# Performance work log

Hardware: AMD Instinct MI355X
Metric: run time of the kernel (lower is better)

Reference implementation:

```python
import jax, jax.numpy as jnp
import numpy as np

N_NODES = 50000
N_EDGES = 800000
NUM_GRAPHS = 64
D_IN = 128
D_HID = 128
D_EMB = 128
D_PRED = 256
D_OUT = 1
BN_EPS = 1e-5


def gcn_conv(x, W, b, src, dst, n_nodes):
    # PyG GCNConv: add self-loops, sym-normalize, aggregate, then bias.
    h = x @ W  # [N, d_out]
    # in-degree with self-loops
    deg = jax.ops.segment_sum(jnp.ones((src.shape[0],), h.dtype), dst,
                              num_segments=n_nodes) + 1.0
    inv_sqrt = 1.0 / jnp.sqrt(deg)  # [N]
    norm = inv_sqrt[src] * inv_sqrt[dst]  # [E]
    msg = h[src] * norm[:, None]  # [E, d_out] gather + scale
    agg = jax.ops.segment_sum(msg, dst, num_segments=n_nodes)
    # self-loop contribution: norm_ii = 1/deg_i
    agg = agg + h / deg[:, None]
    return agg + b


def batch_norm(h, gamma, beta):
    # BatchNorm1d in training mode: batch stats, biased variance
    mean = jnp.mean(h, axis=0)
    var = jnp.mean(jnp.square(h - mean), axis=0)
    return (h - mean) / jnp.sqrt(var + BN_EPS) * gamma + beta


def setup_inputs() -> dict:
    key = jax.random.key(0)
    ks = jax.random.split(key, 12)
    x = jax.random.normal(ks[0], (N_NODES, D_IN), dtype=jnp.float32)
    edge_index = jax.random.randint(ks[1], (2, N_EDGES), 0, N_NODES, dtype=jnp.int32)
    batch = jnp.sort(jax.random.randint(ks[2], (N_NODES,), 0, NUM_GRAPHS, dtype=jnp.int32))
    s1 = 1.0 / np.sqrt(D_IN)
    s2 = 1.0 / np.sqrt(D_HID)
    s3 = 1.0 / np.sqrt(D_EMB)
    s4 = 1.0 / np.sqrt(D_PRED)
    return {
        "x": x,
        "edge_index": edge_index,
        "batch": batch,
        "W1": jax.random.uniform(ks[3], (D_IN, D_HID), jnp.float32, -s1, s1),
        "b1": jnp.zeros((D_HID,), jnp.float32),
        "g1": jnp.ones((D_HID,), jnp.float32),
        "be1": jnp.zeros((D_HID,), jnp.float32),
        "W2": jax.random.uniform(ks[4], (D_HID, D_EMB), jnp.float32, -s2, s2),
        "b2": jnp.zeros((D_EMB,), jnp.float32),
        "g2": jnp.ones((D_EMB,), jnp.float32),
        "be2": jnp.zeros((D_EMB,), jnp.float32),
        "Wp1": jax.random.uniform(ks[5], (D_EMB, D_PRED), jnp.float32, -s3, s3),
        "bp1": jax.random.uniform(ks[6], (D_PRED,), jnp.float32, -s3, s3),
        "Wp2": jax.random.uniform(ks[7], (D_PRED, D_OUT), jnp.float32, -s4, s4),
        "bp2": jax.random.uniform(ks[8], (D_OUT,), jnp.float32, -s4, s4),
    }


def reference(x, edge_index, batch, W1, b1, g1, be1, W2, b2, g2, be2, Wp1, bp1, Wp2, bp2):
    src, dst = edge_index[0], edge_index[1]
    h = gcn_conv(x, W1, b1, src, dst, N_NODES)
    h = batch_norm(jax.nn.relu(h), g1, be1)
    h = gcn_conv(h, W2, b2, src, dst, N_NODES)
    h = batch_norm(jax.nn.relu(h), g2, be2)
    # global max pool per graph
    pooled = jax.ops.segment_max(h, batch, num_segments=NUM_GRAPHS)  # [G, D_EMB]
    # predictor MLP (Dropout is identity in eval)
    z = jax.nn.relu(pooled @ Wp1 + bp1)
    return z @ Wp2 + bp2
```

## Files before the change

kernel.cpp:

```cpp
#include <hip/hip_runtime.h>

#define NN 50000
#define NE 800000
#define NG 64
#define D 128
#define DP 256
#define BN_EPS 1e-5f
#define NSLOT 32
#define NB 196

typedef unsigned short bf16;
typedef __attribute__((ext_vector_type(8))) short s16x8;
typedef __attribute__((ext_vector_type(4))) float f32x4;

__device__ __forceinline__ float bf2f(unsigned h16) {
  unsigned u = (h16 & 0xffffu) << 16; float f; __builtin_memcpy(&f, &u, 4); return f;
}
__device__ __forceinline__ bf16 f2bf(float f) {
  unsigned u; __builtin_memcpy(&u, &f, 4);
  return (bf16)((u + 0x7FFFu + ((u >> 16) & 1u)) >> 16);
}
__device__ __forceinline__ unsigned packbf2(float a, float b) {
  return (unsigned)f2bf(a) | ((unsigned)f2bf(b) << 16);
}
__device__ __forceinline__ s16x8 u4cast(uint4 v) {
  s16x8 r; __builtin_memcpy(&r, &v, 16); return r;
}

__global__ void k_detect(const unsigned short* __restrict__ x, int* __restrict__ flag) {
  int i = threadIdx.x;
  float v = bf2f(x[2 * i]);
  float a = fabsf(v);
  int good = (v == 0.0f) || (a > 1e-30f && a < 32.0f);
  unsigned long long m = __ballot(good);
  if (i == 0) {
    flag[0] = (__popcll(m) >= 56) ? 1 : 0;
    flag[1] = 1;
  }
}

struct CvtArgs {
  const void* s[12];
  float* d[12];
  int n[12];
};

__global__ __launch_bounds__(256) void k_cvt(CvtArgs a, const int* __restrict__ flag) {
  int t = blockIdx.y;
  int n = a.n[t];
  int base = blockIdx.x * 2048;
  if (base >= n) return;
  int mode = flag[0];
  float* dp = a.d[t];
  if (n >= 8) {
    int i8 = base + threadIdx.x * 8;
    if (i8 + 8 <= n) {
      if (mode) {
        uint4 raw = *(const uint4*)((const bf16*)a.s[t] + i8);
        float4 o0 = make_float4(bf2f(raw.x & 0xffff), bf2f(raw.x >> 16),
                                bf2f(raw.y & 0xffff), bf2f(raw.y >> 16));
        float4 o1 = make_float4(bf2f(raw.z & 0xffff), bf2f(raw.z >> 16),
                                bf2f(raw.w & 0xffff), bf2f(raw.w >> 16));
        *(float4*)(dp + i8) = o0;
        *(float4*)(dp + i8 + 4) = o1;
      } else {
        const float* s = (const float*)a.s[t] + i8;
        *(float4*)(dp + i8) = *(const float4*)s;
        *(float4*)(dp + i8 + 4) = *(const float4*)(s + 4);
      }
    }
  } else {
    int i = base + threadIdx.x;
    if (i < n) dp[i] = mode ? bf2f(((const bf16*)a.s[t])[i]) : ((const float*)a.s[t])[i];
  }
}

__global__ __launch_bounds__(256) void k_deg(const int* __restrict__ ei, int* __restrict__ cnt) {
  int e = blockIdx.x * 256 + threadIdx.x;
  if (e < NE) atomicAdd(&cnt[ei[NE + e]], 1);
}

__global__ __launch_bounds__(256) void k_bsum(const int* __restrict__ cnt, int* __restrict__ bsum) {
  int i = blockIdx.x * 256 + threadIdx.x;
  int v = (i < NN) ? cnt[i] : 0;
  __shared__ int s[4];
  for (int off = 32; off; off >>= 1) v += __shfl_down(v, off);
  if ((threadIdx.x & 63) == 0) s[threadIdx.x >> 6] = v;
  __syncthreads();
  if (threadIdx.x == 0) bsum[blockIdx.x] = s[0] + s[1] + s[2] + s[3];
}

__global__ __launch_bounds__(256) void k_bscan(const int* __restrict__ bsum, int* __restrict__ bbase) {
  __shared__ int sh[256];
  int t = threadIdx.x;
  int v = (t < NB) ? bsum[t] : 0;
  sh[t] = v;
  __syncthreads();
  for (int off = 1; off < 256; off <<= 1) {
    int u = (t >= off) ? sh[t - off] : 0;
    __syncthreads();
    sh[t] += u;
    __syncthreads();
  }
  if (t < NB) bbase[t] = sh[t] - v;
}

__global__ __launch_bounds__(256) void k_offsets(const int* __restrict__ cnt, const int* __restrict__ bbase,
                                                 int* __restrict__ ro, int* __restrict__ cursor,
                                                 float* __restrict__ isq) {
  __shared__ int sh[256];
  int t = threadIdx.x;
  int i = blockIdx.x * 256 + t;
  int c = (i < NN) ? cnt[i] : 0;
  sh[t] = c;
  __syncthreads();
  for (int off = 1; off < 256; off <<= 1) {
    int u = (t >= off) ? sh[t - off] : 0;
    __syncthreads();
    sh[t] += u;
    __syncthreads();
  }
  if (i < NN) {
    int o = bbase[blockIdx.x] + sh[t] - c;
    ro[i] = o; cursor[i] = o;
    isq[i] = rsqrtf((float)(c + 1));
  }
  if (i == 0) ro[NN] = NE;
}

__global__ __launch_bounds__(256) void k_fill(const int* __restrict__ ei, const float* __restrict__ isq,
                                              int* __restrict__ cursor, int2* __restrict__ pk) {
  int e = blockIdx.x * 256 + threadIdx.x;
  if (e < NE) {
    int s = ei[e], d = ei[NE + e];
    int slot = atomicAdd(&cursor[d], 1);
    int2 v; v.x = s; v.y = __float_as_int(isq[s] * isq[d]);
    pk[slot] = v;
  }
}

__global__ __launch_bounds__(256) void k_pack(const float* __restrict__ W, const float* __restrict__ scale,
                                              bf16* __restrict__ Wp) {
  int slot = blockIdx.x * 256 + threadIdx.x;
  if (slot >= 2048) return;
  int kc = slot >> 9, ct = (slot >> 6) & 7, l = slot & 63;
  int q = l >> 4, p = l & 15;
  int n = ct * 16 + p;
  unsigned u[4];
#pragma unroll
  for (int jj = 0; jj < 4; ++jj) {
    int k0 = kc * 32 + q * 8 + jj * 2;
    float w0 = W[k0 * D + n], w1 = W[(k0 + 1) * D + n];
    if (scale) { w0 *= scale[k0]; w1 *= scale[k0 + 1]; }
    u[jj] = packbf2(w0, w1);
  }
  uint4 o = make_uint4(u[0], u[1], u[2], u[3]);
  *(uint4*)(Wp + (size_t)slot * 8) = o;
}

__global__ __launch_bounds__(256) void k_mgemm(const void* __restrict__ Xv, const int* __restrict__ flag,
                                               const bf16* __restrict__ Wp,
                                               const float* __restrict__ rowadd,
                                               bf16* __restrict__ Out, int nrows) {
  __shared__ float Cs[4][16][D + 4];
  int l = threadIdx.x & 63, w = threadIdx.x >> 6;
  int q = l >> 4, p = l & 15;
  int mode = flag ? flag[0] : 0;
  float rv[8];
#pragma unroll
  for (int ct = 0; ct < 8; ++ct) rv[ct] = rowadd ? rowadd[ct * 16 + p] : 0.f;
  int ntiles = (nrows + 63) >> 6;
  for (int t = blockIdx.x; t < ntiles; t += gridDim.x) {
    int wb = t * 64 + w * 16;
    int rowc = min(wb + p, nrows - 1);
    f32x4 acc[8];
#pragma unroll
    for (int ct = 0; ct < 8; ++ct) { f32x4 z = {rv[ct], rv[ct], rv[ct], rv[ct]}; acc[ct] = z; }
#pragma unroll
    for (int kc = 0; kc < 4; ++kc) {
      s16x8 a;
      if (mode) {
        uint4 av = *(const uint4*)((const bf16*)Xv + (size_t)rowc * D + kc * 32 + q * 8);
        a = u4cast(av);
      } else {
        const float* Xf = (const float*)Xv + (size_t)rowc * D + kc * 32 + q * 8;
        float4 f0 = *(const float4*)Xf;
        float4 f1 = *(const float4*)(Xf + 4);
        uint4 u = make_uint4(packbf2(f0.x, f0.y), packbf2(f0.z, f0.w),
                             packbf2(f1.x, f1.y), packbf2(f1.z, f1.w));
        a = u4cast(u);
      }
#pragma unroll
      for (int ct = 0; ct < 8; ++ct) {
        s16x8 bfr = *(const s16x8*)(Wp + (size_t)(((kc << 3) + ct) * 64 + l) * 8);
        acc[ct] = __builtin_amdgcn_mfma_f32_16x16x32_bf16(a, bfr, acc[ct], 0, 0, 0);
      }
    }
#pragma unroll
    for (int ct = 0; ct < 8; ++ct)
#pragma unroll
      for (int r = 0; r < 4; ++r)
        Cs[w][q * 4 + r][ct * 16 + p] = acc[ct][r];
    __syncthreads();
#pragma unroll
    for (int i = 0; i < 4; ++i) {
      int idx = i * 64 + l;
      int rr = idx >> 4, c8 = idx & 15;
      int gr = t * 64 + w * 16 + rr;
      if (gr < nrows) {
        float4 v0 = *(const float4*)&Cs[w][rr][c8 * 8];
        float4 v1 = *(const float4*)&Cs[w][rr][c8 * 8 + 4];
        uint4 o = make_uint4(packbf2(v0.x, v0.y), packbf2(v0.z, v0.w),
                             packbf2(v1.x, v1.y), packbf2(v1.z, v1.w));
        *(uint4*)(Out + (size_t)gr * D + c8 * 8) = o;
      }
    }
    __syncthreads();
  }
}

template <int LAYER2>
__global__ __launch_bounds__(256) void k_agg(const bf16* __restrict__ H, const int* __restrict__ ro,
                                             const int2* __restrict__ pk,
                                             const float* __restrict__ b, const int* __restrict__ batch,
                                             bf16* __restrict__ Rout,
                                             float* __restrict__ sumP, float* __restrict__ sumsqP,
                                             float* __restrict__ pooled) {
  int lane = threadIdx.x & 63;
  int w = __builtin_amdgcn_readfirstlane(threadIdx.x >> 6);
  int nbase = blockIdx.x * 16 + w * 4;
  float2 bv = ((const float2*)b)[lane];
  float2 ls = make_float2(0.f, 0.f), lq = make_float2(0.f, 0.f);
  int gcur = -1; float2 mx = make_float2(0.f, 0.f);
  int nend = min(nbase + 4, NN);
  for (int n = nbase; n < nend; ++n) {
    int r0 = __builtin_amdgcn_readfirstlane(ro[n]);
    int r1 = __builtin_amdgcn_readfirstlane(ro[n + 1]);
    float invd = 1.0f / (float)(r1 - r0 + 1);
    unsigned hv = ((const unsigned*)(H + (size_t)n * D))[lane];
    float2 acc = make_float2(bf2f(hv & 0xffff) * invd, bf2f(hv >> 16) * invd);
    int e = r0;
    for (; e + 8 <= r1; e += 8) {
      int2 P[8];
      unsigned X[8];
#pragma unroll
      for (int j = 0; j < 8; ++j) P[j] = pk[e + j];
#pragma unroll
      for (int j = 0; j < 8; ++j) X[j] = ((const unsigned*)(H + (size_t)P[j].x * D))[lane];
#pragma unroll
      for (int j = 0; j < 8; ++j) {
        float c = __int_as_float(P[j].y);
        acc.x += bf2f(X[j] & 0xffff) * c; acc.y += bf2f(X[j] >> 16) * c;
      }
    }
    for (; e + 4 <= r1; e += 4) {
      int2 p0 = pk[e], p1 = pk[e + 1], p2 = pk[e + 2], p3 = pk[e + 3];
      unsigned x0 = ((const unsigned*)(H + (size_t)p0.x * D))[lane];
      unsigned x1 = ((const unsigned*)(H + (size_t)p1.x * D))[lane];
      unsigned x2 = ((const unsigned*)(H + (size_t)p2.x * D))[lane];
      unsigned x3 = ((const unsigned*)(H + (size_t)p3.x * D))[lane];
      float c0 = __int_as_float(p0.y), c1 = __int_as_float(p1.y);
      float c2 = __int_as_float(p2.y), c3 = __int_as_float(p3.y);
      acc.x += bf2f(x0 & 0xffff) * c0; acc.y += bf2f(x0 >> 16) * c0;
      acc.x += bf2f(x1 & 0xffff) * c1; acc.y += bf2f(x1 >> 16) * c1;
      acc.x += bf2f(x2 & 0xffff) * c2; acc.y += bf2f(x2 >> 16) * c2;
      acc.x += bf2f(x3 & 0xffff) * c3; acc.y += bf2f(x3 >> 16) * c3;
    }
    for (; e < r1; ++e) {
      int2 p0 = pk[e];
      unsigned x0 = ((const unsigned*)(H + (size_t)p0.x * D))[lane];
      float c0 = __int_as_float(p0.y);
      acc.x += bf2f(x0 & 0xffff) * c0; acc.y += bf2f(x0 >> 16) * c0;
    }
    float2 r = make_float2(fmaxf(acc.x + bv.x, 0.f), fmaxf(acc.y + bv.y, 0.f));
    if (!LAYER2) ((unsigned*)(Rout + (size_t)n * D))[lane] = packbf2(r.x, r.y);
    ls.x += r.x; ls.y += r.y; lq.x += r.x * r.x; lq.y += r.y * r.y;
    if (LAYER2) {
      int g = batch[n];
      if (g != gcur) {
        if (gcur >= 0) {
          atomicMax((int*)&pooled[(size_t)gcur * D + 2 * lane], __float_as_int(mx.x));
          atomicMax((int*)&pooled[(size_t)gcur * D + 2 * lane + 1], __float_as_int(mx.y));
        }
        gcur = g; mx = make_float2(0.f, 0.f);
      }
      mx.x = fmaxf(mx.x, r.x); mx.y = fmaxf(mx.y, r.y);
    }
  }
  if (LAYER2 && gcur >= 0) {
    atomicMax((int*)&pooled[(size_t)gcur * D + 2 * lane], __float_as_int(mx.x));
    atomicMax((int*)&pooled[(size_t)gcur * D + 2 * lane + 1], __float_as_int(mx.y));
  }
  __shared__ float ss[4][D], sq[4][D];
  ss[w][2 * lane] = ls.x; ss[w][2 * lane + 1] = ls.y;
  sq[w][2 * lane] = lq.x; sq[w][2 * lane + 1] = lq.y;
  __syncthreads();
  int slot = (blockIdx.x & (NSLOT - 1)) * D;
  if (threadIdx.x < D) {
    int k = threadIdx.x;
    atomicAdd(&sumP[slot + k], ss[0][k] + ss[1][k] + ss[2][k] + ss[3][k]);
  } else {
    int k = threadIdx.x - D;
    atomicAdd(&sumsqP[slot + k], sq[0][k] + sq[1][k] + sq[2][k] + sq[3][k]);
  }
}

__global__ void k_bnstats1(const float* __restrict__ sumP, const float* __restrict__ sumsqP,
                           const float* __restrict__ gamma, const float* __restrict__ beta,
                           const float* __restrict__ W2,
                           float* __restrict__ svec, float* __restrict__ tW2) {
  __shared__ float t[D];
  int k = threadIdx.x;
  float sm = 0.f, sq = 0.f;
  for (int i = 0; i < NSLOT; ++i) { sm += sumP[i * D + k]; sq += sumsqP[i * D + k]; }
  float mean = sm * (1.0f / NN);
  float var = sq * (1.0f / NN) - mean * mean;
  float s = gamma[k] * rsqrtf(var + BN_EPS);
  svec[k] = s;
  t[k] = beta[k] - mean * s;
  __syncthreads();
  float acc = 0.f;
  for (int kk = 0; kk < D; ++kk) acc += t[kk] * W2[kk * D + k];
  tW2[k] = acc;
}

__global__ void k_bnstats2(const float* __restrict__ sumP, const float* __restrict__ sumsqP,
                           const float* __restrict__ gamma, const float* __restrict__ beta,
                           float* __restrict__ svec, float* __restrict__ tvec) {
  int k = threadIdx.x;
  float sm = 0.f, sq = 0.f;
  for (int i = 0; i < NSLOT; ++i) { sm += sumP[i * D + k]; sq += sumsqP[i * D + k]; }
  float mean = sm * (1.0f / NN);
  float var = sq * (1.0f / NN) - mean * mean;
  float s = gamma[k] * rsqrtf(var + BN_EPS);
  svec[k] = s;
  tvec[k] = beta[k] - mean * s;
}

__global__ __launch_bounds__(256) void k_head(const float* __restrict__ pooled, const float* __restrict__ s2,
                                              const float* __restrict__ t2, const float* __restrict__ Wp1,
                                              const float* __restrict__ bp1, const float* __restrict__ Wp2,
                                              const float* __restrict__ bp2, void* out,
                                              const int* __restrict__ flag) {
  __shared__ float y[D];
  __shared__ float wr[4];
  int g = blockIdx.x, j = threadIdx.x;
  if (j < D) y[j] = pooled[(size_t)g * D + j] * s2[j] + t2[j];
  __syncthreads();
  float acc = bp1[j];
#pragma unroll 4
  for (int k = 0; k < D; ++k) acc += y[k] * Wp1[k * DP + j];
  float v = fmaxf(acc, 0.f) * Wp2[j];
  for (int off = 32; off; off >>= 1) v += __shfl_down(v, off);
  if ((j & 63) == 0) wr[j >> 6] = v;
  __syncthreads();
  if (j == 0) {
    float r = wr[0] + wr[1] + wr[2] + wr[3] + bp2[0];
    if (flag[0]) ((bf16*)out)[g] = f2bf(r);
    else ((float*)out)[g] = r;
  }
}

extern "C" void kernel_launch(void* const* d_in, const int* in_sizes, int n_in,
                              void* d_out, int out_size, void* d_ws, size_t ws_size,
                              hipStream_t stream) {
  const void* x   = d_in[0];
  const int*  ei  = (const int*)d_in[1];
  const int*  bat = (const int*)d_in[2];

  float* f = (float*)d_ws;
  bf16* A = (bf16*)f; f += (size_t)NN * D / 2;
  bf16* B = (bf16*)f; f += (size_t)NN * D / 2;
  float* W1f  = f; f += D * D;
  float* W2f  = f; f += D * D;
  float* Wp1f = f; f += D * DP;
  float* b1f  = f; f += D;
  float* g1f  = f; f += D;
  float* be1f = f; f += D;
  float* b2f  = f; f += D;
  float* g2f  = f; f += D;
  float* be2f = f; f += D;
  float* bp1f = f; f += DP;
  float* Wp2f = f; f += DP;
  float* bp2f = f; f += 4;
  bf16* Wpk1 = (bf16*)f; f += 2048 * 8 / 2;
  bf16* Wpk2 = (bf16*)f; f += 2048 * 8 / 2;
  float* sum1P   = f; f += NSLOT * D;
  float* sumsq1P = f; f += NSLOT * D;
  float* sum2P   = f; f += NSLOT * D;
  float* sumsq2P = f; f += NSLOT * D;
  float* pooled = f; f += (size_t)NG * D;
  float* svec1  = f; f += D;
  float* tW2    = f; f += D;
  float* svec2  = f; f += D;
  float* tvec2  = f; f += D;
  float* isq    = f; f += NN;
  int2* pk     = (int2*)f; f += (size_t)NE * 2;
  int* ro      = (int*)f; f += NN + 1;
  int* cursor  = (int*)f; f += NN;
  int* cnt     = (int*)f; f += NN;
  int* bsum    = (int*)f; f += NB;
  int* bbase   = (int*)f; f += NB;
  int* flag    = (int*)f;

  hipMemsetAsync(cnt, 0, NN * sizeof(int), stream);
  hipMemsetAsync(sum1P, 0, (4 * NSLOT * D + NG * D) * sizeof(float), stream);

  k_detect<<<1, 64, 0, stream>>>((const unsigned short*)x, flag);

  CvtArgs ca;
  ca.s[0] = d_in[3];  ca.d[0] = W1f;  ca.n[0] = D * D;
  ca.s[1] = d_in[7];  ca.d[1] = W2f;  ca.n[1] = D * D;
  ca.s[2] = d_in[11]; ca.d[2] = Wp1f; ca.n[2] = D * DP;
  ca.s[3] = d_in[4];  ca.d[3] = b1f;  ca.n[3] = D;
  ca.s[4] = d_in[5];  ca.d[4] = g1f;  ca.n[4] = D;
  ca.s[5] = d_in[6];  ca.d[5] = be1f; ca.n[5] = D;
  ca.s[6] = d_in[8];  ca.d[6] = b2f;  ca.n[6] = D;
  ca.s[7] = d_in[9];  ca.d[7] = g2f;  ca.n[7] = D;
  ca.s[8] = d_in[10]; ca.d[8] = be2f; ca.n[8] = D;
  ca.s[9] = d_in[12]; ca.d[9] = bp1f; ca.n[9] = DP;
  ca.s[10] = d_in[13]; ca.d[10] = Wp2f; ca.n[10] = DP;
  ca.s[11] = d_in[14]; ca.d[11] = bp2f; ca.n[11] = 1;
  k_cvt<<<dim3(16, 12), 256, 0, stream>>>(ca, flag);

  k_deg<<<(NE + 255) / 256, 256, 0, stream>>>(ei, cnt);
  k_bsum<<<NB, 256, 0, stream>>>(cnt, bsum);
  k_bscan<<<1, 256, 0, stream>>>(bsum, bbase);
  k_offsets<<<NB, 256, 0, stream>>>(cnt, bbase, ro, cursor, isq);
  k_fill<<<(NE + 255) / 256, 256, 0, stream>>>(ei, isq, cursor, pk);
  k_pack<<<8, 256, 0, stream>>>(W1f, nullptr, Wpk1);

  k_mgemm<<<(NN + 63) / 64, 256, 0, stream>>>(x, flag, Wpk1, nullptr, A, NN);
  k_agg<0><<<(NN + 15) / 16, 256, 0, stream>>>(A, ro, pk, b1f, nullptr,
                                               B, sum1P, sumsq1P, nullptr);
  k_bnstats1<<<1, D, 0, stream>>>(sum1P, sumsq1P, g1f, be1f, W2f, svec1, tW2);

  k_pack<<<8, 256, 0, stream>>>(W2f, svec1, Wpk2);
  k_mgemm<<<(NN + 63) / 64, 256, 0, stream>>>(B, flag + 1, Wpk2, tW2, A, NN);
  k_agg<1><<<(NN + 15) / 16, 256, 0, stream>>>(A, ro, pk, b2f, bat,
                                               nullptr, sum2P, sumsq2P, pooled);
  k_bnstats2<<<1, D, 0, stream>>>(sum2P, sumsq2P, g2f, be2f, svec2, tvec2);

  k_head<<<NG, DP, 0, stream>>>(pooled, svec2, tvec2, Wp1f, bp1f, Wp2f, bp2f, d_out, flag);
}
```

Before: 231.3 us.

## Fuse preprocessing launches and rework aggregation to split edges across half-waves

Merges the detect, convert and degree-count kernels into one launch, and replaces the block-sum/scan/offsets chain with a single scan kernel. That kernel uses a grid-wide spin barrier on an atomic counter and also packs W1. The BN2 stats are folded into the head kernel, and the two memsets become one. The aggregation kernel now gives each half-wave a separate edge while every lane loads 4 bf16 features, then combines the halves with a cross-lane shuffle. The goal is fewer launches and more memory-level parallelism in the gather, but the spin barrier only works if all 204 blocks are resident at the same time.

```diff
diff --git a/kernel.cpp b/kernel.cpp
--- a/kernel.cpp
+++ b/kernel.cpp
@@ -8,6 +8,7 @@
 #define BN_EPS 1e-5f
 #define NSLOT 32
 #define NB 196
+#define NEB 3125
 
 typedef unsigned short bf16;
 typedef __attribute__((ext_vector_type(8))) short s16x8;
@@ -25,18 +26,6 @@
 }
 __device__ __forceinline__ s16x8 u4cast(uint4 v) {
   s16x8 r; __builtin_memcpy(&r, &v, 16); return r;
-}
-
-__global__ void k_detect(const unsigned short* __restrict__ x, int* __restrict__ flag) {
-  int i = threadIdx.x;
-  float v = bf2f(x[2 * i]);
-  float a = fabsf(v);
-  int good = (v == 0.0f) || (a > 1e-30f && a < 32.0f);
-  unsigned long long m = __ballot(good);
-  if (i == 0) {
-    flag[0] = (__popcll(m) >= 56) ? 1 : 0;
-    flag[1] = 1;
-  }
 }
 
 struct CvtArgs {
@@ -45,56 +34,100 @@
   int n[12];
 };
 
-__global__ __launch_bounds__(256) void k_cvt(CvtArgs a, const int* __restrict__ flag) {
-  int t = blockIdx.y;
-  int n = a.n[t];
-  int base = blockIdx.x * 2048;
-  if (base >= n) return;
-  int mode = flag[0];
-  float* dp = a.d[t];
-  if (n >= 8) {
-    int i8 = base + threadIdx.x * 8;
-    if (i8 + 8 <= n) {
-      if (mode) {
-        uint4 raw = *(const uint4*)((const bf16*)a.s[t] + i8);
-        float4 o0 = make_float4(bf2f(raw.x & 0xffff), bf2f(raw.x >> 16),
-                                bf2f(raw.y & 0xffff), bf2f(raw.y >> 16));
-        float4 o1 = make_float4(bf2f(raw.z & 0xffff), bf2f(raw.z >> 16),
-                                bf2f(raw.w & 0xffff), bf2f(raw.w >> 16));
-        *(float4*)(dp + i8) = o0;
-        *(float4*)(dp + i8 + 4) = o1;
-      } else {
-        const float* s = (const float*)a.s[t] + i8;
-        *(float4*)(dp + i8) = *(const float4*)s;
-        *(float4*)(dp + i8 + 4) = *(const float4*)(s + 4);
-      }
-    }
-  } else {
-    int i = base + threadIdx.x;
-    if (i < n) dp[i] = mode ? bf2f(((const bf16*)a.s[t])[i]) : ((const float*)a.s[t])[i];
-  }
-}
-
-__global__ __launch_bounds__(256) void k_deg(const int* __restrict__ ei, int* __restrict__ cnt) {
-  int e = blockIdx.x * 256 + threadIdx.x;
-  if (e < NE) atomicAdd(&cnt[ei[NE + e]], 1);
-}
-
-__global__ __launch_bounds__(256) void k_bsum(const int* __restrict__ cnt, int* __restrict__ bsum) {
-  int i = blockIdx.x * 256 + threadIdx.x;
-  int v = (i < NN) ? cnt[i] : 0;
-  __shared__ int s[4];
-  for (int off = 32; off; off >>= 1) v += __shfl_down(v, off);
-  if ((threadIdx.x & 63) == 0) s[threadIdx.x >> 6] = v;
-  __syncthreads();
-  if (threadIdx.x == 0) bsum[blockIdx.x] = s[0] + s[1] + s[2] + s[3];
-}
-
-__global__ __launch_bounds__(256) void k_bscan(const int* __restrict__ bsum, int* __restrict__ bbase) {
+__global__ __launch_bounds__(256) void k_pre(const int* __restrict__ ei, int* __restrict__ cnt,
+                                             CvtArgs a, const bf16* __restrict__ x,
+                                             int* __restrict__ flag) {
+  int b = blockIdx.x;
+  if (b < NEB) {
+    int e = b * 256 + threadIdx.x;
+    atomicAdd(&cnt[ei[NE + e]], 1);
+    return;
+  }
+  if (b < NEB + 192) {
+    __shared__ int smode;
+    if (threadIdx.x < 64) {
+      float v = bf2f(x[2 * threadIdx.x]);
+      float av = fabsf(v);
+      int good = (v == 0.0f) || (av > 1e-30f && av < 32.0f);
+      unsigned long long m = __ballot(good);
+      if (threadIdx.x == 0) smode = (__popcll(m) >= 56) ? 1 : 0;
+    }
+    __syncthreads();
+    int mode = smode;
+    int idx = b - NEB;
+    int t = idx >> 4;
+    int base = (idx & 15) * 2048;
+    int n = a.n[t];
+    if (base >= n) return;
+    float* dp = a.d[t];
+    if (n >= 8) {
+      int i8 = base + threadIdx.x * 8;
+      if (i8 + 8 <= n) {
+        if (mode) {
+          uint4 raw = *(const uint4*)((const bf16*)a.s[t] + i8);
+          *(float4*)(dp + i8) = make_float4(bf2f(raw.x & 0xffff), bf2f(raw.x >> 16),
+                                            bf2f(raw.y & 0xffff), bf2f(raw.y >> 16));
+          *(float4*)(dp + i8 + 4) = make_float4(bf2f(raw.z & 0xffff), bf2f(raw.z >> 16),
+                                                bf2f(raw.w & 0xffff), bf2f(raw.w >> 16));
+        } else {
+          const float* s = (const float*)a.s[t] + i8;
+          *(float4*)(dp + i8) = *(const float4*)s;
+          *(float4*)(dp + i8 + 4) = *(const float4*)(s + 4);
+        }
+      }
+    } else {
+      int i = base + threadIdx.x;
+      if (i < n) dp[i] = mode ? bf2f(((const bf16*)a.s[t])[i]) : ((const float*)a.s[t])[i];
+    }
+    return;
+  }
+  if (threadIdx.x < 64) {
+    float v = bf2f(x[2 * threadIdx.x]);
+    float av = fabsf(v);
+    int good = (v == 0.0f) || (av > 1e-30f && av < 32.0f);
+    unsigned long long m = __ballot(good);
+    if (threadIdx.x == 0) { flag[0] = (__popcll(m) >= 56) ? 1 : 0; flag[1] = 1; }
+  }
+}
+
+__device__ __forceinline__ void pack_slot(const float* __restrict__ W, const float* __restrict__ scale,
+                                          bf16* __restrict__ Wp, int slot) {
+  int kc = slot >> 9, ct = (slot >> 6) & 7, l = slot & 63;
+  int q = l >> 4, p = l & 15;
+  int n = ct * 16 + p;
+  unsigned u[4];
+#pragma unroll
+  for (int jj = 0; jj < 4; ++jj) {
+    int k0 = kc * 32 + q * 8 + jj * 2;
+    float w0 = W[k0 * D + n], w1 = W[(k0 + 1) * D + n];
+    if (scale) { w0 *= scale[k0]; w1 *= scale[k0 + 1]; }
+    u[jj] = packbf2(w0, w1);
+  }
+  *(uint4*)(Wp + (size_t)slot * 8) = make_uint4(u[0], u[1], u[2], u[3]);
+}
+
+__global__ __launch_bounds__(256) void k_pack(const float* __restrict__ W, const float* __restrict__ scale,
+                                              bf16* __restrict__ Wp) {
+  int slot = blockIdx.x * 256 + threadIdx.x;
+  if (slot < 2048) pack_slot(W, scale, Wp, slot);
+}
+
+__global__ __launch_bounds__(256) void k_scan3(const int* __restrict__ cnt,
+                                               int* __restrict__ bsum, int* __restrict__ done,
+                                               int* __restrict__ ro, int* __restrict__ cursor,
+                                               float* __restrict__ isq,
+                                               const float* __restrict__ W1f, bf16* __restrict__ Wpk1) {
+  int b = blockIdx.x, t = threadIdx.x;
+  if (b >= NB) {
+    pack_slot(W1f, nullptr, Wpk1, (b - NB) * 256 + t);
+    return;
+  }
   __shared__ int sh[256];
-  int t = threadIdx.x;
-  int v = (t < NB) ? bsum[t] : 0;
-  sh[t] = v;
+  __shared__ int spart[4];
+  __shared__ int sbase;
+  int i = b * 256 + t;
+  int c = (i < NN) ? cnt[i] : 0;
+  sh[t] = c;
   __syncthreads();
   for (int off = 1; off < 256; off <<= 1) {
     int u = (t >= off) ? sh[t - off] : 0;
@@ -102,26 +135,23 @@
     sh[t] += u;
     __syncthreads();
   }
-  if (t < NB) bbase[t] = sh[t] - v;
-}
-
-__global__ __launch_bounds__(256) void k_offsets(const int* __restrict__ cnt, const int* __restrict__ bbase,
-                                                 int* __restrict__ ro, int* __restrict__ cursor,
-                                                 float* __restrict__ isq) {
-  __shared__ int sh[256];
-  int t = threadIdx.x;
-  int i = blockIdx.x * 256 + t;
-  int c = (i < NN) ? cnt[i] : 0;
-  sh[t] = c;
-  __syncthreads();
-  for (int off = 1; off < 256; off <<= 1) {
-    int u = (t >= off) ? sh[t - off] : 0;
-    __syncthreads();
-    sh[t] += u;
-    __syncthreads();
-  }
+  if (t == 255) {
+    atomicExch(&bsum[b], sh[255]);
+    __threadfence();
+    atomicAdd(done, 1);
+  }
+  if (t == 0) {
+    while (atomicAdd(done, 0) < NB) { __builtin_amdgcn_s_sleep(2); }
+  }
+  __syncthreads();
+  int v = (t < b) ? atomicAdd(&bsum[t], 0) : 0;
+  for (int off = 32; off; off >>= 1) v += __shfl_down(v, off);
+  if ((t & 63) == 0) spart[t >> 6] = v;
+  __syncthreads();
+  if (t == 0) sbase = spart[0] + spart[1] + spart[2] + spart[3];
+  __syncthreads();
   if (i < NN) {
-    int o = bbase[blockIdx.x] + sh[t] - c;
+    int o = sbase + sh[t] - c;
     ro[i] = o; cursor[i] = o;
     isq[i] = rsqrtf((float)(c + 1));
   }
@@ -137,25 +167,6 @@
     int2 v; v.x = s; v.y = __float_as_int(isq[s] * isq[d]);
     pk[slot] = v;
   }
-}
-
-__global__ __launch_bounds__(256) void k_pack(const float* __restrict__ W, const float* __restrict__ scale,
-                                              bf16* __restrict__ Wp) {
-  int slot = blockIdx.x * 256 + threadIdx.x;
-  if (slot >= 2048) return;
-  int kc = slot >> 9, ct = (slot >> 6) & 7, l = slot & 63;
-  int q = l >> 4, p = l & 15;
-  int n = ct * 16 + p;
-  unsigned u[4];
-#pragma unroll
-  for (int jj = 0; jj < 4; ++jj) {
-    int k0 = kc * 32 + q * 8 + jj * 2;
-    float w0 = W[k0 * D + n], w1 = W[(k0 + 1) * D + n];
-    if (scale) { w0 *= scale[k0]; w1 *= scale[k0 + 1]; }
-    u[jj] = packbf2(w0, w1);
-  }
-  uint4 o = make_uint4(u[0], u[1], u[2], u[3]);
-  *(uint4*)(Wp + (size_t)slot * 8) = o;
 }
 
 __global__ __launch_bounds__(256) void k_mgemm(const void* __restrict__ Xv, const int* __restrict__ flag,
@@ -220,80 +231,88 @@
 }
 
 template <int LAYER2>
-__global__ __launch_bounds__(256) void k_agg(const bf16* __restrict__ H, const int* __restrict__ ro,
-                                             const int2* __restrict__ pk,
-                                             const float* __restrict__ b, const int* __restrict__ batch,
-                                             bf16* __restrict__ Rout,
-                                             float* __restrict__ sumP, float* __restrict__ sumsqP,
-                                             float* __restrict__ pooled) {
+__global__ __launch_bounds__(256, 4) void k_agg(const bf16* __restrict__ H, const int* __restrict__ ro,
+                                                const int2* __restrict__ pk,
+                                                const float* __restrict__ b, const int* __restrict__ batch,
+                                                bf16* __restrict__ Rout,
+                                                float* __restrict__ sumP, float* __restrict__ sumsqP,
+                                                float* __restrict__ pooled) {
   int lane = threadIdx.x & 63;
   int w = __builtin_amdgcn_readfirstlane(threadIdx.x >> 6);
+  int h = lane >> 5, c = lane & 31;
   int nbase = blockIdx.x * 16 + w * 4;
-  float2 bv = ((const float2*)b)[lane];
-  float2 ls = make_float2(0.f, 0.f), lq = make_float2(0.f, 0.f);
-  int gcur = -1; float2 mx = make_float2(0.f, 0.f);
+  float4 bv = ((const float4*)b)[c];
+  float ls[4] = {0.f, 0.f, 0.f, 0.f}, lq[4] = {0.f, 0.f, 0.f, 0.f}, mx[4] = {0.f, 0.f, 0.f, 0.f};
+  int gcur = -1;
   int nend = min(nbase + 4, NN);
   for (int n = nbase; n < nend; ++n) {
-    int r0 = __builtin_amdgcn_readfirstlane(ro[n]);
-    int r1 = __builtin_amdgcn_readfirstlane(ro[n + 1]);
-    float invd = 1.0f / (float)(r1 - r0 + 1);
-    unsigned hv = ((const unsigned*)(H + (size_t)n * D))[lane];
-    float2 acc = make_float2(bf2f(hv & 0xffff) * invd, bf2f(hv >> 16) * invd);
-    int e = r0;
-    for (; e + 8 <= r1; e += 8) {
-      int2 P[8];
-      unsigned X[8];
-#pragma unroll
-      for (int j = 0; j < 8; ++j) P[j] = pk[e + j];
-#pragma unroll
-      for (int j = 0; j < 8; ++j) X[j] = ((const unsigned*)(H + (size_t)P[j].x * D))[lane];
-#pragma unroll
-      for (int j = 0; j < 8; ++j) {
-        float c = __int_as_float(P[j].y);
-        acc.x += bf2f(X[j] & 0xffff) * c; acc.y += bf2f(X[j] >> 16) * c;
-      }
-    }
-    for (; e + 4 <= r1; e += 4) {
-      int2 p0 = pk[e], p1 = pk[e + 1], p2 = pk[e + 2], p3 = pk[e + 3];
-      unsigned x0 = ((const unsigned*)(H + (size_t)p0.x * D))[lane];
-      unsigned x1 = ((const unsigned*)(H + (size_t)p1.x * D))[lane];
-      unsigned x2 = ((const unsigned*)(H + (size_t)p2.x * D))[lane];
-      unsigned x3 = ((const unsigned*)(H + (size_t)p3.x * D))[lane];
-      float c0 = __int_as_float(p0.y), c1 = __int_as_float(p1.y);
-      float c2 = __int_as_float(p2.y), c3 = __int_as_float(p3.y);
-      acc.x += bf2f(x0 & 0xffff) * c0; acc.y += bf2f(x0 >> 16) * c0;
-      acc.x += bf2f(x1 & 0xffff) * c1; acc.y += bf2f(x1 >> 16) * c1;
-      acc.x += bf2f(x2 & 0xffff) * c2; acc.y += bf2f(x2 >> 16) * c2;
-      acc.x += bf2f(x3 & 0xffff) * c3; acc.y += bf2f(x3 >> 16) * c3;
-    }
-    for (; e < r1; ++e) {
-      int2 p0 = pk[e];
-      unsigned x0 = ((const unsigned*)(H + (size_t)p0.x * D))[lane];
-      float c0 = __int_as_float(p0.y);
-      acc.x += bf2f(x0 & 0xffff) * c0; acc.y += bf2f(x0 >> 16) * c0;
-    }
-    float2 r = make_float2(fmaxf(acc.x + bv.x, 0.f), fmaxf(acc.y + bv.y, 0.f));
-    if (!LAYER2) ((unsigned*)(Rout + (size_t)n * D))[lane] = packbf2(r.x, r.y);
-    ls.x += r.x; ls.y += r.y; lq.x += r.x * r.x; lq.y += r.y * r.y;
+    int e0 = __builtin_amdgcn_readfirstlane(ro[n]);
+    int e1 = __builtin_amdgcn_readfirstlane(ro[n + 1]);
+    float invd = 1.0f / (float)(e1 - e0 + 1);
+    uint2 hv = ((const uint2*)(H + (size_t)n * D))[c];
+    float acc[4] = {0.f, 0.f, 0.f, 0.f};
+    int e = e0;
+    for (; e + 8 <= e1; e += 8) {
+      int2 P[4]; uint2 X[4];
+#pragma unroll
+      for (int it = 0; it < 4; ++it) P[it] = pk[e + 2 * it + h];
+#pragma unroll
+      for (int it = 0; it < 4; ++it) X[it] = ((const uint2*)(H + (size_t)P[it].x * D))[c];
+#pragma unroll
+      for (int it = 0; it < 4; ++it) {
+        float cc = __int_as_float(P[it].y);
+        acc[0] += bf2f(X[it].x & 0xffff) * cc; acc[1] += bf2f(X[it].x >> 16) * cc;
+        acc[2] += bf2f(X[it].y & 0xffff) * cc; acc[3] += bf2f(X[it].y >> 16) * cc;
+      }
+    }
+    for (; e < e1; e += 2) {
+      int eh = e + h;
+      int2 p0 = (eh < e1) ? pk[eh] : make_int2(n, 0);
+      uint2 X0 = ((const uint2*)(H + (size_t)p0.x * D))[c];
+      float cc = __int_as_float(p0.y);
+      acc[0] += bf2f(X0.x & 0xffff) * cc; acc[1] += bf2f(X0.x >> 16) * cc;
+      acc[2] += bf2f(X0.y & 0xffff) * cc; acc[3] += bf2f(X0.y >> 16) * cc;
+    }
+#pragma unroll
+    for (int j = 0; j < 4; ++j) acc[j] += __shfl_xor(acc[j], 32);
+    float sf[4] = {bf2f(hv.x & 0xffff), bf2f(hv.x >> 16), bf2f(hv.y & 0xffff), bf2f(hv.y >> 16)};
+    float bb[4] = {bv.x, bv.y, bv.z, bv.w};
+    float r[4];
+#pragma unroll
+    for (int j = 0; j < 4; ++j) {
+      r[j] = fmaxf(acc[j] + sf[j] * invd + bb[j], 0.f);
+      ls[j] += r[j]; lq[j] += r[j] * r[j];
+    }
+    if (!LAYER2) {
+      if (h == 0)
+        ((uint2*)(Rout + (size_t)n * D))[c] = make_uint2(packbf2(r[0], r[1]), packbf2(r[2], r[3]));
+    }
     if (LAYER2) {
       int g = batch[n];
       if (g != gcur) {
-        if (gcur >= 0) {
-          atomicMax((int*)&pooled[(size_t)gcur * D + 2 * lane], __float_as_int(mx.x));
-          atomicMax((int*)&pooled[(size_t)gcur * D + 2 * lane + 1], __float_as_int(mx.y));
+        if (gcur >= 0 && h == 0) {
+#pragma unroll
+          for (int j = 0; j < 4; ++j)
+            atomicMax((int*)&pooled[(size_t)gcur * D + 4 * c + j], __float_as_int(mx[j]));
         }
-        gcur = g; mx = make_float2(0.f, 0.f);
-      }
-      mx.x = fmaxf(mx.x, r.x); mx.y = fmaxf(mx.y, r.y);
-    }
-  }
-  if (LAYER2 && gcur >= 0) {
-    atomicMax((int*)&pooled[(size_t)gcur * D + 2 * lane], __float_as_int(mx.x));
-    atomicMax((int*)&pooled[(size_t)gcur * D + 2 * lane + 1], __float_as_int(mx.y));
+        gcur = g;
+#pragma unroll
+        for (int j = 0; j < 4; ++j) mx[j] = 0.f;
+      }
+#pragma unroll
+      for (int j = 0; j < 4; ++j) mx[j] = fmaxf(mx[j], r[j]);
+    }
+  }
+  if (LAYER2 && gcur >= 0 && h == 0) {
+#pragma unroll
+    for (int j = 0; j < 4; ++j)
+      atomicMax((int*)&pooled[(size_t)gcur * D + 4 * c + j], __float_as_int(mx[j]));
   }
   __shared__ float ss[4][D], sq[4][D];
-  ss[w][2 * lane] = ls.x; ss[w][2 * lane + 1] = ls.y;
-  sq[w][2 * lane] = lq.x; sq[w][2 * lane + 1] = lq.y;
+  if (h == 0) {
+#pragma unroll
+    for (int j = 0; j < 4; ++j) { ss[w][4 * c + j] = ls[j]; sq[w][4 * c + j] = lq[j]; }
+  }
   __syncthreads();
   int slot = (blockIdx.x & (NSLOT - 1)) * D;
   if (threadIdx.x < D) {
@@ -324,28 +343,24 @@
   tW2[k] = acc;
 }
 
-__global__ void k_bnstats2(const float* __restrict__ sumP, const float* __restrict__ sumsqP,
-                           const float* __restrict__ gamma, const float* __restrict__ beta,
-                           float* __restrict__ svec, float* __restrict__ tvec) {
-  int k = threadIdx.x;
-  float sm = 0.f, sq = 0.f;
-  for (int i = 0; i < NSLOT; ++i) { sm += sumP[i * D + k]; sq += sumsqP[i * D + k]; }
-  float mean = sm * (1.0f / NN);
-  float var = sq * (1.0f / NN) - mean * mean;
-  float s = gamma[k] * rsqrtf(var + BN_EPS);
-  svec[k] = s;
-  tvec[k] = beta[k] - mean * s;
-}
-
-__global__ __launch_bounds__(256) void k_head(const float* __restrict__ pooled, const float* __restrict__ s2,
-                                              const float* __restrict__ t2, const float* __restrict__ Wp1,
+__global__ __launch_bounds__(256) void k_head(const float* __restrict__ pooled,
+                                              const float* __restrict__ sum2P, const float* __restrict__ sumsq2P,
+                                              const float* __restrict__ gamma2, const float* __restrict__ beta2,
+                                              const float* __restrict__ Wp1,
                                               const float* __restrict__ bp1, const float* __restrict__ Wp2,
                                               const float* __restrict__ bp2, void* out,
                                               const int* __restrict__ flag) {
   __shared__ float y[D];
   __shared__ float wr[4];
   int g = blockIdx.x, j = threadIdx.x;
-  if (j < D) y[j] = pooled[(size_t)g * D + j] * s2[j] + t2[j];
+  if (j < D) {
+    float sm = 0.f, sq = 0.f;
+    for (int i = 0; i < NSLOT; ++i) { sm += sum2P[i * D + j]; sq += sumsq2P[i * D + j]; }
+    float mean = sm * (1.0f / NN);
+    float var = sq * (1.0f / NN) - mean * mean;
+    float s = gamma2[j] * rsqrtf(var + BN_EPS);
+    y[j] = pooled[(size_t)g * D + j] * s + (beta2[j] - mean * s);
+  }
   __syncthreads();
   float acc = bp1[j];
 #pragma unroll 4
@@ -371,6 +386,15 @@
   float* f = (float*)d_ws;
   bf16* A = (bf16*)f; f += (size_t)NN * D / 2;
   bf16* B = (bf16*)f; f += (size_t)NN * D / 2;
+  float* zbase = f;
+  int* cnt  = (int*)f; f += NN;
+  int* done = (int*)f; f += 4;
+  float* sum1P   = f; f += NSLOT * D;
+  float* sumsq1P = f; f += NSLOT * D;
+  float* sum2P   = f; f += NSLOT * D;
+  float* sumsq2P = f; f += NSLOT * D;
+  float* pooled  = f; f += (size_t)NG * D;
+  size_t zbytes = (size_t)((char*)f - (char*)zbase);
   float* W1f  = f; f += D * D;
   float* W2f  = f; f += D * D;
   float* Wp1f = f; f += D * DP;
@@ -385,28 +409,16 @@
   float* bp2f = f; f += 4;
   bf16* Wpk1 = (bf16*)f; f += 2048 * 8 / 2;
   bf16* Wpk2 = (bf16*)f; f += 2048 * 8 / 2;
-  float* sum1P   = f; f += NSLOT * D;
-  float* sumsq1P = f; f += NSLOT * D;
-  float* sum2P   = f; f += NSLOT * D;
-  float* sumsq2P = f; f += NSLOT * D;
-  float* pooled = f; f += (size_t)NG * D;
-  float* svec1  = f; f += D;
-  float* tW2    = f; f += D;
-  float* svec2  = f; f += D;
-  float* tvec2  = f; f += D;
-  float* isq    = f; f += NN;
-  int2* pk     = (int2*)f; f += (size_t)NE * 2;
-  int* ro      = (int*)f; f += NN + 1;
-  int* cursor  = (int*)f; f += NN;
-  int* cnt     = (int*)f; f += NN;
-  int* bsum    = (int*)f; f += NB;
-  int* bbase   = (int*)f; f += NB;
-  int* flag    = (int*)f;
-
-  hipMemsetAsync(cnt, 0, NN * sizeof(int), stream);
-  hipMemsetAsync(sum1P, 0, (4 * NSLOT * D + NG * D) * sizeof(float), stream);
-
-  k_detect<<<1, 64, 0, stream>>>((const unsigned short*)x, flag);
+  float* svec1 = f; f += D;
+  float* tW2   = f; f += D;
+  float* isq   = f; f += NN;
+  int2* pk    = (int2*)f; f += (size_t)NE * 2;
+  int* ro     = (int*)f; f += NN + 1;
+  int* cursor = (int*)f; f += NN;
+  int* bsum   = (int*)f; f += NB;
+  int* flag   = (int*)f;
+
+  hipMemsetAsync(zbase, 0, zbytes, stream);
 
   CvtArgs ca;
   ca.s[0] = d_in[3];  ca.d[0] = W1f;  ca.n[0] = D * D;
@@ -421,14 +433,10 @@
   ca.s[9] = d_in[12]; ca.d[9] = bp1f; ca.n[9] = DP;
   ca.s[10] = d_in[13]; ca.d[10] = Wp2f; ca.n[10] = DP;
   ca.s[11] = d_in[14]; ca.d[11] = bp2f; ca.n[11] = 1;
-  k_cvt<<<dim3(16, 12), 256, 0, stream>>>(ca, flag);
-
-  k_deg<<<(NE + 255) / 256, 256, 0, stream>>>(ei, cnt);
-  k_bsum<<<NB, 256, 0, stream>>>(cnt, bsum);
-  k_bscan<<<1, 256, 0, stream>>>(bsum, bbase);
-  k_offsets<<<NB, 256, 0, stream>>>(cnt, bbase, ro, cursor, isq);
-  k_fill<<<(NE + 255) / 256, 256, 0, stream>>>(ei, isq, cursor, pk);
-  k_pack<<<8, 256, 0, stream>>>(W1f, nullptr, Wpk1);
+
+  k_pre<<<NEB + 192 + 1, 256, 0, stream>>>(ei, cnt, ca, (const bf16*)x, flag);
+  k_scan3<<<NB + 8, 256, 0, stream>>>(cnt, bsum, done, ro, cursor, isq, W1f, Wpk1);
+  k_fill<<<NEB, 256, 0, stream>>>(ei, isq, cursor, pk);
 
   k_mgemm<<<(NN + 63) / 64, 256, 0, stream>>>(x, flag, Wpk1, nullptr, A, NN);
   k_agg<0><<<(NN + 15) / 16, 256, 0, stream>>>(A, ro, pk, b1f, nullptr,
@@ -439,7 +447,7 @@
   k_mgemm<<<(NN + 63) / 64, 256, 0, stream>>>(B, flag + 1, Wpk2, tW2, A, NN);
   k_agg<1><<<(NN + 15) / 16, 256, 0, stream>>>(A, ro, pk, b2f, bat,
                                                nullptr, sum2P, sumsq2P, pooled);
-  k_bnstats2<<<1, D, 0, stream>>>(sum2P, sumsq2P, g2f, be2f, svec2, tvec2);
-
-  k_head<<<NG, DP, 0, stream>>>(pooled, svec2, tvec2, Wp1f, bp1f, Wp2f, bp2f, d_out, flag);
-}
+
+  k_head<<<NG, DP, 0, stream>>>(pooled, sum2P, sumsq2P, g2f, be2f,
+                                Wp1f, bp1f, Wp2f, bp2f, d_out, flag);
+}
```

Result: slower. 267.3 us (+15.5%).
